# Performance work log

Measured on AMD Instinct MI355X. Metric: run time of the kernel, lower is better.

The kernel has to match this reference:

```python
import jax, jax.numpy as jnp
import numpy as np

BZ, IN_DIM, STATE_DIM, OUT_DIM, L = 16, 512, 512, 512, 2048
INIT_SCALE = 0.5


def setup_inputs() -> dict:
    key = jax.random.key(0)
    k_u, k_a, k_b, k_c = jax.random.split(key, 4)
    u = jax.random.normal(k_u, (BZ, IN_DIM, L), dtype=jnp.float32)
    A_unconstrained = jax.random.normal(k_a, (STATE_DIM,), dtype=jnp.float32) * 0.1
    B = jax.random.normal(k_b, (STATE_DIM, IN_DIM), dtype=jnp.float32) * INIT_SCALE / np.sqrt(IN_DIM)
    C = jax.random.normal(k_c, (OUT_DIM, STATE_DIM), dtype=jnp.float32) * INIT_SCALE / np.sqrt(STATE_DIM)
    D = jnp.zeros((OUT_DIM, IN_DIM), dtype=jnp.float32)
    h0 = jnp.zeros((STATE_DIM,), dtype=jnp.float32)
    return {"u": u, "A_unconstrained": A_unconstrained, "B": B, "C": C, "D": D, "h0": h0}


def reference(u, A_unconstrained, B, C, D, h0):
    # u: (Bz, input_dim, L)
    Bz = u.shape[0]
    A_diag = -jax.nn.softplus(A_unconstrained)  # (S,)
    # Time-invariant input projection, batched over all timesteps: (L, Bz, S)
    Bu = jnp.einsum('bil,si->lbs', u, B)

    state0 = jnp.broadcast_to(h0[None, :], (Bz, h0.shape[0]))

    def step(state, bu_t):
        x_t = state * A_diag[None, :] + bu_t  # (Bz, S)
        return x_t, x_t

    _, xs = jax.lax.scan(step, state0, Bu)  # xs: (L, Bz, S)

    # Output projection: y_t = C x_t + D u_t  -> (Bz, out, L)
    Y = jnp.einsum('lbs,os->bol', xs, C) + jnp.einsum('bil,oi->bol', u, D)
    return Y
```

## Files before the change

kernel.cpp:

```cpp
#include <hip/hip_runtime.h>
#include <math.h>

typedef __bf16 bf16;
typedef __bf16 bf16x2 __attribute__((ext_vector_type(2)));
typedef __bf16 bf16x4 __attribute__((ext_vector_type(4)));
typedef __bf16 bf16x8 __attribute__((ext_vector_type(8)));
typedef float  f32x4  __attribute__((ext_vector_type(4)));

#define BZd 16
#define INd 512
#define Sd  512
#define Od  512
#define Ld  2048
#define CLd 128
#define NCd (Ld / CLd)

__device__ __forceinline__ int keyf(int r) { return (r & 3) ^ ((r >> 2) & 3); }

__global__ __launch_bounds__(256) void prep_all(const float* __restrict__ B,
                                                const float* __restrict__ C,
                                                const float* __restrict__ D,
                                                const float* __restrict__ Au,
                                                bf16* __restrict__ Bb, bf16* __restrict__ Cb,
                                                bf16* __restrict__ Db, float* __restrict__ A_diag,
                                                int* __restrict__ dfa) {
    __shared__ int sred[4];
    int bid = blockIdx.x;
    if (bid == 768) {
        #pragma unroll
        for (int r = 0; r < 2; ++r) {
            int ss = threadIdx.x + r * 256;
            float x = Au[ss];
            float sp = fmaxf(x, 0.0f) + log1pf(expf(-fabsf(x)));
            A_diag[ss] = -sp;
        }
        return;
    }
    int which = bid >> 8, lb = bid & 255;
    const float* src = which == 0 ? B : (which == 1 ? C : D);
    bf16* dst = which == 0 ? Bb : (which == 1 ? Cb : Db);
    int i = lb * 256 + threadIdx.x;
    f32x4 v = *(const f32x4*)&src[(size_t)i * 4];
    bf16x4 o = { (bf16)v[0], (bf16)v[1], (bf16)v[2], (bf16)v[3] };
    *(bf16x4*)&dst[(size_t)i * 4] = o;
    if (which == 2) {
        int nz = (v[0] != 0.f) | (v[1] != 0.f) | (v[2] != 0.f) | (v[3] != 0.f);
        unsigned long long bl = __ballot(nz);
        int wv = threadIdx.x >> 6;
        if ((threadIdx.x & 63) == 0) sred[wv] = (bl != 0ull);
        __syncthreads();
        if (threadIdx.x == 0) dfa[lb] = sred[0] | sred[1] | sred[2] | sred[3];
    }
}

__global__ __launch_bounds__(256) void transp_u(const float* __restrict__ u,
                                                bf16* __restrict__ ut) {
    __shared__ bf16 t[64][73];
    int b = blockIdx.z, i0 = blockIdx.y * 64, l0 = blockIdx.x * 64;
    int tid = threadIdx.x, tx = tid & 15, ty = tid >> 4;
    const float* ub = u + ((size_t)b * INd + i0) * Ld + l0;
    #pragma unroll
    for (int r = 0; r < 4; ++r) {
        int il = r * 16 + ty;
        float4 v = *(const float4*)&ub[(size_t)il * Ld + tx * 4];
        t[il][tx * 4 + 0] = (bf16)v.x;
        t[il][tx * 4 + 1] = (bf16)v.y;
        t[il][tx * 4 + 2] = (bf16)v.z;
        t[il][tx * 4 + 3] = (bf16)v.w;
    }
    __syncthreads();
    bf16* uo = ut + ((size_t)b * Ld + l0) * INd + i0;
    #pragma unroll
    for (int it = 0; it < 2; ++it) {
        int q = it * 256 + tid;
        int lr = q >> 3;
        int ic = (q & 7) * 8;
        bf16x8 o;
        #pragma unroll
        for (int e = 0; e < 8; ++e) o[e] = t[ic + e][lr];
        *(bf16x8*)&uo[(size_t)lr * INd + ic] = o;
    }
}

template<int SCAN>
__global__ __launch_bounds__(512, 2) void gemm8p(
    const bf16* __restrict__ Abf, size_t aBS,
    const float* __restrict__ Uf, size_t uBS,
    const bf16* __restrict__ Bbf, size_t bBS,
    const bf16* __restrict__ Dbf,
    const int* __restrict__ dfa,
    const float* __restrict__ A_diag, float* __restrict__ cePtr,
    void* __restrict__ OutV, size_t oBS, int ldOut,
    int NX, int NY)
{
    constexpr int RS   = 32;
    constexpr int ASZ  = 256 * RS;
    constexpr int SLOT = ASZ + 256 * 32;
    __shared__ bf16 lds[4 * SLOT];

    const int tid = threadIdx.x;
    const int lane = tid & 63, w = tid >> 6;

    int nwg = gridDim.x, bid = blockIdx.x;
    int cpx = nwg >> 3;
    int swz = (bid & 7) * cpx + (bid >> 3);
    int pb = NX * NY;
    int b  = swz / pb;
    int r0 = swz - b * pb;
    int by = r0 / NX;
    int bx = r0 - by * NX;

    const int wm = w >> 2, wn = w & 3;
    const int fr = lane & 15, g = lane >> 4;
    const int iq = tid & 7, lq = tid >> 3;

    const bf16*  Ab = Abf + (size_t)b * aBS + (size_t)(by * 256) * 512;
    const float* Ub = Uf ? (Uf + (size_t)b * uBS) : nullptr;
    const bf16*  Bp = Bbf + (size_t)b * bBS + (size_t)(bx * 256) * 512;

    int extra = 0;
    if (!SCAN && dfa) {
        int4 f = ((const int4*)dfa)[lane];
        extra = __any((f.x | f.y | f.z | f.w) != 0) ? 1 : 0;
    }

    f32x4 acc[8][4];
    #pragma unroll
    for (int i = 0; i < 8; ++i)
        #pragma unroll
        for (int j = 0; j < 4; ++j)
            acc[i][j] = (f32x4){0.f, 0.f, 0.f, 0.f};

    #define GLD16(srcP, dstElem) __builtin_amdgcn_global_load_lds( \
        (const __attribute__((address_space(1))) void*)(srcP), \
        (__attribute__((address_space(3))) void*)&lds[dstElem], 16, 0, 0)

    auto gldA = [&](int U) {
        #pragma unroll
        for (int rb = 0; rb < 2; ++rb) {
            int row = rb * 128 + (tid >> 2);
            int cs = (tid & 3) ^ keyf(row);
            GLD16(Ab + (size_t)row * 512 + U * 32 + cs * 8,
                  (U & 3) * SLOT + (rb * 128 + w * 16) * 32);
        }
    };
    auto gldB = [&](int U) {
        #pragma unroll
        for (int rb = 0; rb < 2; ++rb) {
            int row = rb * 128 + (tid >> 2);
            int cs = (tid & 3) ^ keyf(row);
            GLD16(Bp + (size_t)row * 512 + U * 32 + cs * 8,
                  (U & 3) * SLOT + ASZ + (rb * 128 + w * 16) * 32);
        }
    };
    auto readFrags = [&](int slot, bf16x8* avf, bf16x8* bvf) {
        const bf16* As = &lds[slot * SLOT];
        const bf16* Bs = &lds[slot * SLOT + ASZ];
        #pragma unroll
        for (int i = 0; i < 8; ++i) {
            int R = wm * 128 + i * 16 + fr;
            avf[i] = *(const bf16x8*)&As[R * RS + (g ^ keyf(R)) * 8];
        }
        #pragma unroll
        for (int j = 0; j < 4; ++j) {
            int R = wn * 64 + j * 16 + fr;
            bvf[j] = *(const bf16x8*)&Bs[R * 32 + (g ^ keyf(R)) * 8];
        }
    };

    gldA(0); gldB(0); gldA(1); gldB(1);

    for (int U = 0; U < 16; ++U) {
        if (U < 15) { asm volatile("s_waitcnt vmcnt(4)" ::: "memory"); }
        else        { asm volatile("s_waitcnt vmcnt(0)" ::: "memory"); }
        __builtin_amdgcn_sched_barrier(0);
        __builtin_amdgcn_s_barrier();
        __builtin_amdgcn_sched_barrier(0);
        bf16x8 av[8], bv[4];
        readFrags(U & 3, av, bv);
        if (U + 2 < 16) gldA(U + 2);
        if (U + 2 < 16) gldB(U + 2);
        __builtin_amdgcn_s_setprio(1);
        #pragma unroll
        for (int i = 0; i < 8; ++i)
            #pragma unroll
            for (int j = 0; j < 4; ++j)
                acc[i][j] = __builtin_amdgcn_mfma_f32_16x16x32_bf16(av[i], bv[j], acc[i][j], 0, 0, 0);
        __builtin_amdgcn_s_setprio(0);
    }

    if (!SCAN && extra) {
        #pragma unroll 1
        for (int T = 0; T < 16; ++T) {
            int k0 = T * 32;
            __builtin_amdgcn_s_barrier();
            f32x4 r4[4];
            #pragma unroll
            for (int d = 0; d < 4; ++d)
                r4[d] = *(const f32x4*)&Ub[(size_t)(k0 + iq * 4 + d) * Ld + bx * 256 + lq * 4];
            #pragma unroll
            for (int rb = 0; rb < 2; ++rb) {
                int row = rb * 128 + (tid >> 2);
                int cs = (tid & 3) ^ keyf(row);
                GLD16(Dbf + (size_t)(by * 256 + row) * 512 + k0 + cs * 8,
                      (rb * 128 + w * 16) * 32);
            }
            asm volatile("s_waitcnt vmcnt(0)" ::: "memory");
            #pragma unroll
            for (int dl = 0; dl < 4; ++dl) {
                int r = lq * 4 + dl;
                bf16x4 wv = { (bf16)r4[0][dl], (bf16)r4[1][dl], (bf16)r4[2][dl], (bf16)r4[3][dl] };
                int e = ((iq >> 1) ^ keyf(r)) * 8 + (iq & 1) * 4;
                *(bf16x4*)&lds[ASZ + r * 32 + e] = wv;
            }
            asm volatile("s_waitcnt lgkmcnt(0)" ::: "memory");
            __builtin_amdgcn_s_barrier();
            bf16x8 av[8], bv[4];
            readFrags(0, av, bv);
            #pragma unroll
            for (int i = 0; i < 8; ++i)
                #pragma unroll
                for (int j = 0; j < 4; ++j)
                    acc[i][j] = __builtin_amdgcn_mfma_f32_16x16x32_bf16(av[i], bv[j], acc[i][j], 0, 0, 0);
        }
    }

    int n0 = bx * 256 + wn * 64 + fr;
    int m0 = by * 256 + wm * 128 + g * 4;

    if (SCAN) {
        #pragma unroll
        for (int j = 0; j < 4; ++j) {
            float a = A_diag[n0 + j * 16];
            float a2 = a * a, a4 = a2 * a2, a8 = a4 * a4, a16 = a8 * a8;
            float S = 0.f;
            #pragma unroll
            for (int i = 0; i < 8; ++i) {
                f32x4 v = acc[i][j];
                float e = fmaf(fmaf(fmaf(v[0], a, v[1]), a, v[2]), a, v[3]);
                float e0 = __shfl(e, fr), e1 = __shfl(e, fr + 16);
                float e2 = __shfl(e, fr + 32), e3 = __shfl(e, fr + 48);
                float E = fmaf(fmaf(fmaf(e0, a4, e1), a4, e2), a4, e3);
                S = fmaf(S, a16, E);
            }
            if (g == 0)
                cePtr[((size_t)b * NCd + (by * 2 + wm)) * Sd + n0 + j * 16] = S;
        }
    }

    if (SCAN) {
        bf16* out = (bf16*)OutV + (size_t)b * oBS;
        #pragma unroll
        for (int i = 0; i < 8; ++i)
            #pragma unroll
            for (int j = 0; j < 4; ++j)
                #pragma unroll
                for (int q = 0; q < 4; ++q)
                    out[(size_t)(m0 + i * 16 + q) * ldOut + n0 + j * 16] = (bf16)acc[i][j][q];
    } else {
        float* out = (float*)OutV + (size_t)b * oBS;
        #pragma unroll
        for (int i = 0; i < 8; ++i)
            #pragma unroll
            for (int j = 0; j < 4; ++j)
                #pragma unroll
                for (int q = 0; q < 4; ++q)
                    out[(size_t)(m0 + i * 16 + q) * ldOut + n0 + j * 16] = acc[i][j][q];
    }
    #undef GLD16
}

__global__ __launch_bounds__(256) void pass_scan2(bf16* __restrict__ xbuf,
                                                  const float* __restrict__ A_diag,
                                                  const float* __restrict__ ce,
                                                  const float* __restrict__ h0) {
    int gI = blockIdx.x * 256 + threadIdx.x;
    int sp = gI & 255;
    int c = (gI >> 8) & (NCd - 1);
    int b = gI >> 12;
    int s = sp * 2;
    float a0 = A_diag[s], a1 = A_diag[s + 1];
    float acl0 = a0, acl1 = a1;
    #pragma unroll
    for (int i = 0; i < 7; ++i) { acl0 *= acl0; acl1 *= acl1; }
    float x0 = h0[s], x1 = h0[s + 1];
    for (int cp = 0; cp < NCd; ++cp) {
        if (cp >= c) break;
        float2 e = *(const float2*)&ce[((size_t)b * NCd + cp) * Sd + s];
        x0 = fmaf(acl0, x0, e.x);
        x1 = fmaf(acl1, x1, e.y);
    }
    bf16* p = xbuf + ((size_t)b * Ld + (size_t)c * CLd) * Sd + s;
    #pragma unroll 4
    for (int j = 0; j < CLd; ++j) {
        bf16x2 v = *(const bf16x2*)&p[(size_t)j * Sd];
        x0 = fmaf(a0, x0, (float)v[0]);
        x1 = fmaf(a1, x1, (float)v[1]);
        bf16x2 o = { (bf16)x0, (bf16)x1 };
        *(bf16x2*)&p[(size_t)j * Sd] = o;
    }
}

extern "C" void kernel_launch(void* const* d_in, const int* in_sizes, int n_in,
                              void* d_out, int out_size, void* d_ws, size_t ws_size,
                              hipStream_t stream) {
    const float* u  = (const float*)d_in[0];
    const float* Au = (const float*)d_in[1];
    const float* Bm = (const float*)d_in[2];
    const float* Cm = (const float*)d_in[3];
    const float* Dm = (const float*)d_in[4];
    const float* h0 = (const float*)d_in[5];
    float* Y = (float*)d_out;

    char* ws = (char*)d_ws;
    bf16* xs = (bf16*)ws;
    bf16* ut = (bf16*)(ws + (32ull << 20));
    bf16* Bb = (bf16*)(ws + (64ull << 20));
    bf16* Cb = Bb + 262144;
    bf16* Db = Cb + 262144;
    float* A_diag = (float*)(ws + (64ull << 20) + 3ull * 524288);
    float* ce     = A_diag + 512;
    int*   dfa    = (int*)(ce + (size_t)BZd * NCd * Sd);

    prep_all<<<769, 256, 0, stream>>>(Bm, Cm, Dm, Au, Bb, Cb, Db, A_diag, dfa);
    transp_u<<<dim3(Ld / 64, INd / 64, BZd), 256, 0, stream>>>(u, ut);

    gemm8p<1><<<(Sd / 256) * (Ld / 256) * BZd, 512, 0, stream>>>(
        ut, (size_t)Ld * INd, nullptr, 0, Bb, 0, nullptr,
        nullptr, A_diag, ce,
        (void*)xs, (size_t)Ld * Sd, Sd,
        Sd / 256, Ld / 256);

    pass_scan2<<<(BZd * NCd * (Sd / 2)) / 256, 256, 0, stream>>>(xs, A_diag, ce, h0);

    gemm8p<0><<<(Ld / 256) * (Od / 256) * BZd, 512, 0, stream>>>(
        Cb, 0, u, (size_t)INd * Ld, xs, (size_t)Ld * Sd, Db,
        dfa, A_diag, nullptr,
        (void*)Y, (size_t)Od * Ld, Ld,
        Ld / 256, Od / 256);
}
```

Measured before the change: 94.35 us.

## Fuse prep, transpose, input GEMM and scan into one cooperative kernel

The weight-conversion, u transpose, input-projection GEMM and chunked scan kernels are merged into a single cooperative kernel of 256 workgroups, separated by grid-wide syncs. This removes three kernel launches and their inter-kernel gaps. Each workgroup now handles a strided set of transpose tiles, one GEMM tile, and one scan slice. The output GEMM is specialised with hardcoded dimensions. The cost is that grid syncs serialise the phases, and the scan phase runs only 256 threads per workgroup, which gives less parallelism than the old separate scan kernel.

```diff
diff --git a/kernel.cpp b/kernel.cpp
--- a/kernel.cpp
+++ b/kernel.cpp
@@ -1,5 +1,8 @@
 #include <hip/hip_runtime.h>
+#include <hip/hip_cooperative_groups.h>
 #include <math.h>
+
+namespace cg = cooperative_groups;
 
 typedef __bf16 bf16;
 typedef __bf16 bf16x2 __attribute__((ext_vector_type(2)));
@@ -17,85 +20,236 @@
 
 __device__ __forceinline__ int keyf(int r) { return (r & 3) ^ ((r >> 2) & 3); }
 
-__global__ __launch_bounds__(256) void prep_all(const float* __restrict__ B,
-                                                const float* __restrict__ C,
-                                                const float* __restrict__ D,
-                                                const float* __restrict__ Au,
-                                                bf16* __restrict__ Bb, bf16* __restrict__ Cb,
-                                                bf16* __restrict__ Db, float* __restrict__ A_diag,
-                                                int* __restrict__ dfa) {
-    __shared__ int sred[4];
-    int bid = blockIdx.x;
-    if (bid == 768) {
-        #pragma unroll
-        for (int r = 0; r < 2; ++r) {
-            int ss = threadIdx.x + r * 256;
-            float x = Au[ss];
-            float sp = fmaxf(x, 0.0f) + log1pf(expf(-fabsf(x)));
-            A_diag[ss] = -sp;
-        }
-        return;
-    }
-    int which = bid >> 8, lb = bid & 255;
-    const float* src = which == 0 ? B : (which == 1 ? C : D);
-    bf16* dst = which == 0 ? Bb : (which == 1 ? Cb : Db);
-    int i = lb * 256 + threadIdx.x;
-    f32x4 v = *(const f32x4*)&src[(size_t)i * 4];
-    bf16x4 o = { (bf16)v[0], (bf16)v[1], (bf16)v[2], (bf16)v[3] };
-    *(bf16x4*)&dst[(size_t)i * 4] = o;
-    if (which == 2) {
+__global__ __launch_bounds__(512, 2) void fused_front(
+    const float* __restrict__ u, const float* __restrict__ Au,
+    const float* __restrict__ Bm, const float* __restrict__ Cm,
+    const float* __restrict__ Dm, const float* __restrict__ h0,
+    bf16* __restrict__ ut, bf16* __restrict__ Bb, bf16* __restrict__ Cb,
+    bf16* __restrict__ Db, float* __restrict__ A_diag, int* __restrict__ dfa,
+    float* __restrict__ ce, bf16* __restrict__ xs)
+{
+    constexpr int RS = 32, ASZ = 256 * RS, SLOT = ASZ + 256 * 32;
+    __shared__ bf16 lds[4 * SLOT];
+    __shared__ int sred[8];
+
+    const int tid = threadIdx.x, bid = blockIdx.x;
+    cg::grid_group gridg = cg::this_grid();
+
+    if (bid < 128) {
+        int unit = bid * 512 + tid;
+        {
+            f32x4 v = *(const f32x4*)&Bm[(size_t)unit * 4];
+            bf16x4 o = { (bf16)v[0], (bf16)v[1], (bf16)v[2], (bf16)v[3] };
+            *(bf16x4*)&Bb[(size_t)unit * 4] = o;
+        }
+        f32x4 v = *(const f32x4*)&Dm[(size_t)unit * 4];
+        bf16x4 o = { (bf16)v[0], (bf16)v[1], (bf16)v[2], (bf16)v[3] };
+        *(bf16x4*)&Db[(size_t)unit * 4] = o;
         int nz = (v[0] != 0.f) | (v[1] != 0.f) | (v[2] != 0.f) | (v[3] != 0.f);
         unsigned long long bl = __ballot(nz);
-        int wv = threadIdx.x >> 6;
-        if ((threadIdx.x & 63) == 0) sred[wv] = (bl != 0ull);
+        if ((tid & 63) == 0) sred[tid >> 6] = (bl != 0ull);
         __syncthreads();
-        if (threadIdx.x == 0) dfa[lb] = sred[0] | sred[1] | sred[2] | sred[3];
+        if (tid == 0)
+            dfa[bid] = sred[0] | sred[1] | sred[2] | sred[3] |
+                       sred[4] | sred[5] | sred[6] | sred[7];
+    } else {
+        int unit = (bid - 128) * 512 + tid;
+        f32x4 v = *(const f32x4*)&Cm[(size_t)unit * 4];
+        bf16x4 o = { (bf16)v[0], (bf16)v[1], (bf16)v[2], (bf16)v[3] };
+        *(bf16x4*)&Cb[(size_t)unit * 4] = o;
+        if (tid == 0) dfa[bid] = 0;
+        if (bid == 255) {
+            float x = Au[tid];
+            A_diag[tid] = -(fmaxf(x, 0.0f) + log1pf(expf(-fabsf(x))));
+        }
+    }
+    __syncthreads();
+
+    {
+        bf16* tb = lds + (tid >> 8) * (64 * 73);
+        int stid = tid & 255;
+        int tx = stid & 15, ty = stid >> 4;
+        #pragma unroll 1
+        for (int it = 0; it < 8; ++it) {
+            int T = bid * 16 + it * 2 + (tid >> 8);
+            int b = T >> 8, rem = T & 255;
+            int i0 = (rem >> 5) * 64, l0 = (rem & 31) * 64;
+            const float* ub = u + ((size_t)b * INd + i0) * Ld + l0;
+            __syncthreads();
+            #pragma unroll
+            for (int r = 0; r < 4; ++r) {
+                int il = r * 16 + ty;
+                f32x4 v = *(const f32x4*)&ub[(size_t)il * Ld + tx * 4];
+                tb[il * 73 + tx * 4 + 0] = (bf16)v[0];
+                tb[il * 73 + tx * 4 + 1] = (bf16)v[1];
+                tb[il * 73 + tx * 4 + 2] = (bf16)v[2];
+                tb[il * 73 + tx * 4 + 3] = (bf16)v[3];
+            }
+            __syncthreads();
+            bf16* uo = ut + ((size_t)b * Ld + l0) * INd + i0;
+            #pragma unroll
+            for (int q2 = 0; q2 < 2; ++q2) {
+                int q = q2 * 256 + stid;
+                int lr = q >> 3;
+                int ic = (q & 7) * 8;
+                bf16x8 o;
+                #pragma unroll
+                for (int e = 0; e < 8; ++e) o[e] = tb[(ic + e) * 73 + lr];
+                *(bf16x8*)&uo[(size_t)lr * INd + ic] = o;
+            }
+        }
+    }
+
+    gridg.sync();
+
+    const int lane = tid & 63, w = tid >> 6;
+    int cpx = 256 >> 3;
+    int swz = (bid & 7) * cpx + (bid >> 3);
+    int b  = swz / 16;
+    int r0 = swz - b * 16;
+    int by = r0 >> 1;
+    int bx = r0 & 1;
+
+    const int wm = w >> 2, wn = w & 3;
+    const int fr = lane & 15, g = lane >> 4;
+
+    {
+        const bf16* Ab = ut + (size_t)b * Ld * INd + (size_t)(by * 256) * 512;
+        const bf16* Bp = Bb + (size_t)(bx * 256) * 512;
+
+        f32x4 acc[8][4];
+        #pragma unroll
+        for (int i = 0; i < 8; ++i)
+            #pragma unroll
+            for (int j = 0; j < 4; ++j)
+                acc[i][j] = (f32x4){0.f, 0.f, 0.f, 0.f};
+
+        #define GLD16(srcP, dstElem) __builtin_amdgcn_global_load_lds( \
+            (const __attribute__((address_space(1))) void*)(srcP), \
+            (__attribute__((address_space(3))) void*)&lds[dstElem], 16, 0, 0)
+
+        auto gldA = [&](int U) {
+            #pragma unroll
+            for (int rb = 0; rb < 2; ++rb) {
+                int row = rb * 128 + (tid >> 2);
+                int cs = (tid & 3) ^ keyf(row);
+                GLD16(Ab + (size_t)row * 512 + U * 32 + cs * 8,
+                      (U & 3) * SLOT + (rb * 128 + w * 16) * 32);
+            }
+        };
+        auto gldB = [&](int U) {
+            #pragma unroll
+            for (int rb = 0; rb < 2; ++rb) {
+                int row = rb * 128 + (tid >> 2);
+                int cs = (tid & 3) ^ keyf(row);
+                GLD16(Bp + (size_t)row * 512 + U * 32 + cs * 8,
+                      (U & 3) * SLOT + ASZ + (rb * 128 + w * 16) * 32);
+            }
+        };
+
+        gldA(0); gldB(0); gldA(1); gldB(1);
+
+        for (int U = 0; U < 16; ++U) {
+            if (U < 15) { asm volatile("s_waitcnt vmcnt(4)" ::: "memory"); }
+            else        { asm volatile("s_waitcnt vmcnt(0)" ::: "memory"); }
+            __builtin_amdgcn_sched_barrier(0);
+            __builtin_amdgcn_s_barrier();
+            __builtin_amdgcn_sched_barrier(0);
+            bf16x8 av[8], bv[4];
+            {
+                const bf16* As = &lds[(U & 3) * SLOT];
+                const bf16* Bs = &lds[(U & 3) * SLOT + ASZ];
+                #pragma unroll
+                for (int i = 0; i < 8; ++i) {
+                    int R = wm * 128 + i * 16 + fr;
+                    av[i] = *(const bf16x8*)&As[R * RS + (g ^ keyf(R)) * 8];
+                }
+                #pragma unroll
+                for (int j = 0; j < 4; ++j) {
+                    int R = wn * 64 + j * 16 + fr;
+                    bv[j] = *(const bf16x8*)&Bs[R * 32 + (g ^ keyf(R)) * 8];
+                }
+            }
+            if (U + 2 < 16) gldA(U + 2);
+            if (U + 2 < 16) gldB(U + 2);
+            __builtin_amdgcn_s_setprio(1);
+            #pragma unroll
+            for (int i = 0; i < 8; ++i)
+                #pragma unroll
+                for (int j = 0; j < 4; ++j)
+                    acc[i][j] = __builtin_amdgcn_mfma_f32_16x16x32_bf16(av[i], bv[j], acc[i][j], 0, 0, 0);
+            __builtin_amdgcn_s_setprio(0);
+        }
+        #undef GLD16
+
+        int n0 = bx * 256 + wn * 64 + fr;
+        int m0 = by * 256 + wm * 128 + g * 4;
+
+        #pragma unroll
+        for (int j = 0; j < 4; ++j) {
+            float a = A_diag[n0 + j * 16];
+            float a2 = a * a, a4 = a2 * a2, a8 = a4 * a4, a16 = a8 * a8;
+            float S = 0.f;
+            #pragma unroll
+            for (int i = 0; i < 8; ++i) {
+                f32x4 v = acc[i][j];
+                float e = fmaf(fmaf(fmaf(v[0], a, v[1]), a, v[2]), a, v[3]);
+                float e0 = __shfl(e, fr), e1 = __shfl(e, fr + 16);
+                float e2 = __shfl(e, fr + 32), e3 = __shfl(e, fr + 48);
+                float E = fmaf(fmaf(fmaf(e0, a4, e1), a4, e2), a4, e3);
+                S = fmaf(S, a16, E);
+            }
+            if (g == 0)
+                ce[((size_t)b * NCd + (by * 2 + wm)) * Sd + n0 + j * 16] = S;
+        }
+
+        bf16* out = xs + (size_t)b * Ld * Sd;
+        #pragma unroll
+        for (int i = 0; i < 8; ++i)
+            #pragma unroll
+            for (int j = 0; j < 4; ++j)
+                #pragma unroll
+                for (int q = 0; q < 4; ++q)
+                    out[(size_t)(m0 + i * 16 + q) * Sd + n0 + j * 16] = (bf16)acc[i][j][q];
+    }
+
+    gridg.sync();
+
+    if (tid < 256) {
+        int c  = by * 2 + (tid >> 7);
+        int sp = bx * 128 + (tid & 127);
+        int s  = sp * 2;
+        float a0 = A_diag[s], a1 = A_diag[s + 1];
+        float acl0 = a0, acl1 = a1;
+        #pragma unroll
+        for (int i = 0; i < 7; ++i) { acl0 *= acl0; acl1 *= acl1; }
+        float x0 = h0[s], x1 = h0[s + 1];
+        for (int cp = 0; cp < c; ++cp) {
+            float2 e = *(const float2*)&ce[((size_t)b * NCd + cp) * Sd + s];
+            x0 = fmaf(acl0, x0, e.x);
+            x1 = fmaf(acl1, x1, e.y);
+        }
+        bf16* p = xs + ((size_t)b * Ld + (size_t)c * CLd) * Sd + s;
+        #pragma unroll 4
+        for (int j = 0; j < CLd; ++j) {
+            bf16x2 v = *(const bf16x2*)&p[(size_t)j * Sd];
+            x0 = fmaf(a0, x0, (float)v[0]);
+            x1 = fmaf(a1, x1, (float)v[1]);
+            bf16x2 o = { (bf16)x0, (bf16)x1 };
+            *(bf16x2*)&p[(size_t)j * Sd] = o;
+        }
     }
 }
 
-__global__ __launch_bounds__(256) void transp_u(const float* __restrict__ u,
-                                                bf16* __restrict__ ut) {
-    __shared__ bf16 t[64][73];
-    int b = blockIdx.z, i0 = blockIdx.y * 64, l0 = blockIdx.x * 64;
-    int tid = threadIdx.x, tx = tid & 15, ty = tid >> 4;
-    const float* ub = u + ((size_t)b * INd + i0) * Ld + l0;
-    #pragma unroll
-    for (int r = 0; r < 4; ++r) {
-        int il = r * 16 + ty;
-        float4 v = *(const float4*)&ub[(size_t)il * Ld + tx * 4];
-        t[il][tx * 4 + 0] = (bf16)v.x;
-        t[il][tx * 4 + 1] = (bf16)v.y;
-        t[il][tx * 4 + 2] = (bf16)v.z;
-        t[il][tx * 4 + 3] = (bf16)v.w;
-    }
-    __syncthreads();
-    bf16* uo = ut + ((size_t)b * Ld + l0) * INd + i0;
-    #pragma unroll
-    for (int it = 0; it < 2; ++it) {
-        int q = it * 256 + tid;
-        int lr = q >> 3;
-        int ic = (q & 7) * 8;
-        bf16x8 o;
-        #pragma unroll
-        for (int e = 0; e < 8; ++e) o[e] = t[ic + e][lr];
-        *(bf16x8*)&uo[(size_t)lr * INd + ic] = o;
-    }
-}
-
-template<int SCAN>
-__global__ __launch_bounds__(512, 2) void gemm8p(
-    const bf16* __restrict__ Abf, size_t aBS,
-    const float* __restrict__ Uf, size_t uBS,
-    const bf16* __restrict__ Bbf, size_t bBS,
+__global__ __launch_bounds__(512, 2) void gemm_y256(
+    const bf16* __restrict__ Cb,
+    const float* __restrict__ Uf,
+    const bf16* __restrict__ xs,
     const bf16* __restrict__ Dbf,
     const int* __restrict__ dfa,
-    const float* __restrict__ A_diag, float* __restrict__ cePtr,
-    void* __restrict__ OutV, size_t oBS, int ldOut,
-    int NX, int NY)
+    float* __restrict__ Y)
 {
-    constexpr int RS   = 32;
-    constexpr int ASZ  = 256 * RS;
-    constexpr int SLOT = ASZ + 256 * 32;
+    constexpr int RS = 32, ASZ = 256 * RS, SLOT = ASZ + 256 * 32;
     __shared__ bf16 lds[4 * SLOT];
 
     const int tid = threadIdx.x;
@@ -104,22 +258,21 @@
     int nwg = gridDim.x, bid = blockIdx.x;
     int cpx = nwg >> 3;
     int swz = (bid & 7) * cpx + (bid >> 3);
-    int pb = NX * NY;
-    int b  = swz / pb;
-    int r0 = swz - b * pb;
-    int by = r0 / NX;
-    int bx = r0 - by * NX;
+    int b  = swz / 16;
+    int r0 = swz - b * 16;
+    int by = r0 >> 3;
+    int bx = r0 & 7;
 
     const int wm = w >> 2, wn = w & 3;
     const int fr = lane & 15, g = lane >> 4;
     const int iq = tid & 7, lq = tid >> 3;
 
-    const bf16*  Ab = Abf + (size_t)b * aBS + (size_t)(by * 256) * 512;
-    const float* Ub = Uf ? (Uf + (size_t)b * uBS) : nullptr;
-    const bf16*  Bp = Bbf + (size_t)b * bBS + (size_t)(bx * 256) * 512;
-
-    int extra = 0;
-    if (!SCAN && dfa) {
+    const bf16*  Ab = Cb + (size_t)(by * 256) * 512;
+    const float* Ub = Uf + (size_t)b * INd * Ld;
+    const bf16*  Bp = xs + (size_t)b * Ld * Sd + (size_t)(bx * 256) * 512;
+
+    int extra;
+    {
         int4 f = ((const int4*)dfa)[lane];
         extra = __any((f.x | f.y | f.z | f.w) != 0) ? 1 : 0;
     }
@@ -189,7 +342,7 @@
         __builtin_amdgcn_s_setprio(0);
     }
 
-    if (!SCAN && extra) {
+    if (extra) {
         #pragma unroll 1
         for (int T = 0; T < 16; ++T) {
             int k0 = T * 32;
@@ -224,81 +377,18 @@
                     acc[i][j] = __builtin_amdgcn_mfma_f32_16x16x32_bf16(av[i], bv[j], acc[i][j], 0, 0, 0);
         }
     }
+    #undef GLD16
 
     int n0 = bx * 256 + wn * 64 + fr;
     int m0 = by * 256 + wm * 128 + g * 4;
-
-    if (SCAN) {
-        #pragma unroll
-        for (int j = 0; j < 4; ++j) {
-            float a = A_diag[n0 + j * 16];
-            float a2 = a * a, a4 = a2 * a2, a8 = a4 * a4, a16 = a8 * a8;
-            float S = 0.f;
-            #pragma unroll
-            for (int i = 0; i < 8; ++i) {
-                f32x4 v = acc[i][j];
-                float e = fmaf(fmaf(fmaf(v[0], a, v[1]), a, v[2]), a, v[3]);
-                float e0 = __shfl(e, fr), e1 = __shfl(e, fr + 16);
-                float e2 = __shfl(e, fr + 32), e3 = __shfl(e, fr + 48);
-                float E = fmaf(fmaf(fmaf(e0, a4, e1), a4, e2), a4, e3);
-                S = fmaf(S, a16, E);
-            }
-            if (g == 0)
-                cePtr[((size_t)b * NCd + (by * 2 + wm)) * Sd + n0 + j * 16] = S;
-        }
-    }
-
-    if (SCAN) {
-        bf16* out = (bf16*)OutV + (size_t)b * oBS;
-        #pragma unroll
-        for (int i = 0; i < 8; ++i)
-            #pragma unroll
-            for (int j = 0; j < 4; ++j)
-                #pragma unroll
-                for (int q = 0; q < 4; ++q)
-                    out[(size_t)(m0 + i * 16 + q) * ldOut + n0 + j * 16] = (bf16)acc[i][j][q];
-    } else {
-        float* out = (float*)OutV + (size_t)b * oBS;
-        #pragma unroll
-        for (int i = 0; i < 8; ++i)
-            #pragma unroll
-            for (int j = 0; j < 4; ++j)
-                #pragma unroll
-                for (int q = 0; q < 4; ++q)
-                    out[(size_t)(m0 + i * 16 + q) * ldOut + n0 + j * 16] = acc[i][j][q];
-    }
-    #undef GLD16
-}
-
-__global__ __launch_bounds__(256) void pass_scan2(bf16* __restrict__ xbuf,
-                                                  const float* __restrict__ A_diag,
-                                                  const float* __restrict__ ce,
-                                                  const float* __restrict__ h0) {
-    int gI = blockIdx.x * 256 + threadIdx.x;
-    int sp = gI & 255;
-    int c = (gI >> 8) & (NCd - 1);
-    int b = gI >> 12;
-    int s = sp * 2;
-    float a0 = A_diag[s], a1 = A_diag[s + 1];
-    float acl0 = a0, acl1 = a1;
+    float* out = Y + (size_t)b * Od * Ld;
     #pragma unroll
-    for (int i = 0; i < 7; ++i) { acl0 *= acl0; acl1 *= acl1; }
-    float x0 = h0[s], x1 = h0[s + 1];
-    for (int cp = 0; cp < NCd; ++cp) {
-        if (cp >= c) break;
-        float2 e = *(const float2*)&ce[((size_t)b * NCd + cp) * Sd + s];
-        x0 = fmaf(acl0, x0, e.x);
-        x1 = fmaf(acl1, x1, e.y);
-    }
-    bf16* p = xbuf + ((size_t)b * Ld + (size_t)c * CLd) * Sd + s;
-    #pragma unroll 4
-    for (int j = 0; j < CLd; ++j) {
-        bf16x2 v = *(const bf16x2*)&p[(size_t)j * Sd];
-        x0 = fmaf(a0, x0, (float)v[0]);
-        x1 = fmaf(a1, x1, (float)v[1]);
-        bf16x2 o = { (bf16)x0, (bf16)x1 };
-        *(bf16x2*)&p[(size_t)j * Sd] = o;
-    }
+    for (int i = 0; i < 8; ++i)
+        #pragma unroll
+        for (int j = 0; j < 4; ++j)
+            #pragma unroll
+            for (int q = 0; q < 4; ++q)
+                out[(size_t)(m0 + i * 16 + q) * Ld + n0 + j * 16] = acc[i][j][q];
 }
 
 extern "C" void kernel_launch(void* const* d_in, const int* in_sizes, int n_in,
@@ -322,20 +412,11 @@
     float* ce     = A_diag + 512;
     int*   dfa    = (int*)(ce + (size_t)BZd * NCd * Sd);
 
-    prep_all<<<769, 256, 0, stream>>>(Bm, Cm, Dm, Au, Bb, Cb, Db, A_diag, dfa);
-    transp_u<<<dim3(Ld / 64, INd / 64, BZd), 256, 0, stream>>>(u, ut);
-
-    gemm8p<1><<<(Sd / 256) * (Ld / 256) * BZd, 512, 0, stream>>>(
-        ut, (size_t)Ld * INd, nullptr, 0, Bb, 0, nullptr,
-        nullptr, A_diag, ce,
-        (void*)xs, (size_t)Ld * Sd, Sd,
-        Sd / 256, Ld / 256);
-
-    pass_scan2<<<(BZd * NCd * (Sd / 2)) / 256, 256, 0, stream>>>(xs, A_diag, ce, h0);
-
-    gemm8p<0><<<(Ld / 256) * (Od / 256) * BZd, 512, 0, stream>>>(
-        Cb, 0, u, (size_t)INd * Ld, xs, (size_t)Ld * Sd, Db,
-        dfa, A_diag, nullptr,
-        (void*)Y, (size_t)Od * Ld, Ld,
-        Ld / 256, Od / 256);
+    void* args[] = { (void*)&u, (void*)&Au, (void*)&Bm, (void*)&Cm, (void*)&Dm,
+                     (void*)&h0, (void*)&ut, (void*)&Bb, (void*)&Cb, (void*)&Db,
+                     (void*)&A_diag, (void*)&dfa, (void*)&ce, (void*)&xs };
+    hipLaunchCooperativeKernel((const void*)fused_front, dim3(256), dim3(512),
+                               args, 0, stream);
+
+    gemm_y256<<<256, 512, 0, stream>>>(Cb, u, xs, Db, dfa, Y);
 }
```

Result: slower. 174.3 us (+84.7%).
